# Performance work log

Hardware: AMD Instinct MI355X
Metric: run time of the kernel (lower is better)

Reference implementation:

```python
import jax, jax.numpy as jnp
import numpy as np
import math

IN_F, OUT_F, RANK, ALPHA = 4096, 4096, 16, 32
SCALING = ALPHA / RANK


def setup_inputs() -> dict:
    key = jax.random.key(0)
    k_x, k_w, k_a = jax.random.split(key, 3)
    x = jax.random.normal(k_x, (4, 2048, IN_F), dtype=jnp.float32)
    weight = jax.random.normal(k_w, (OUT_F, IN_F), dtype=jnp.float32)
    bias = jnp.zeros((OUT_F,), dtype=jnp.float32)
    lora_A = jax.random.normal(k_a, (RANK, IN_F), dtype=jnp.float32) * math.sqrt(2.0 / RANK)
    lora_B = jnp.zeros((OUT_F, RANK), dtype=jnp.float32)
    return {"x": x, "weight": weight, "bias": bias, "lora_A": lora_A, "lora_B": lora_B}


def reference(x, weight, bias, lora_A, lora_B):
    # base: x @ W^T + b    [B,S,out]
    base = jnp.einsum("bsi,oi->bso", x, weight) + bias
    # faithful to source: materialize full rank-update matrix (B @ A) [out,in]
    delta_w = lora_B @ lora_A
    lora = jnp.einsum("bsi,oi->bso", x, delta_w) * SCALING
    return base + lora
```

## Files before the change

kernel.cpp:

```cpp
#include <hip/hip_runtime.h>
#include <hip/hip_bf16.h>

#define IN_F   4096
#define OUT_F  4096
#define M_ROWS 8192
#define RANK   16
#define SCALING 2.0f

#define BM 256
#define BN 256
#define BK 64
#define NT (IN_F / BK)

typedef __attribute__((ext_vector_type(8))) short bf16x8;
typedef __attribute__((ext_vector_type(4))) float f32x4;
typedef unsigned short ushort_t;

template<int V> struct ic { static constexpr int value = V; };

__device__ __forceinline__ short f2b(float f) {
    union { float f; unsigned u; } c; c.f = f;
    unsigned r = (c.u + 0x7FFFu + ((c.u >> 16) & 1u)) >> 16;
    return (short)r;
}

__device__ __forceinline__ float4 ld4(const float* p) { return *(const float4*)p; }

__device__ __forceinline__ float4 s4(float4 v, float s) {
    v.x *= s; v.y *= s; v.z *= s; v.w *= s; return v;
}

__device__ __forceinline__ bf16x8 pack8(float4 a, float4 b) {
    bf16x8 r;
    r[0] = f2b(a.x); r[1] = f2b(a.y); r[2] = f2b(a.z); r[3] = f2b(a.w);
    r[4] = f2b(b.x); r[5] = f2b(b.y); r[6] = f2b(b.z); r[7] = f2b(b.w);
    return r;
}

__device__ __forceinline__ void gload16(const void* g, void* l) {
    __builtin_amdgcn_global_load_lds(
        (const __attribute__((address_space(1))) unsigned int*)g,
        (__attribute__((address_space(3))) unsigned int*)l, 16, 0, 0);
}

__global__ __launch_bounds__(256) void cvt3_kernel(const float* __restrict__ x,
                                                   const float* __restrict__ w,
                                                   const float* __restrict__ a,
                                                   ushort_t* __restrict__ xb,
                                                   ushort_t* __restrict__ wb,
                                                   ushort_t* __restrict__ ab) {
    const int n8x = M_ROWS * IN_F / 8;
    const int n8w = OUT_F * IN_F / 8;
    const int n8a = RANK * IN_F / 8;
    const int ntot = n8x + n8w + n8a;
    int i = blockIdx.x * blockDim.x + threadIdx.x;
    const int stride = gridDim.x * blockDim.x;
    for (; i < ntot; i += stride) {
        const float* src; ushort_t* dst; int j;
        if (i < n8x)            { src = x; dst = xb; j = i; }
        else if (i < n8x + n8w) { src = w; dst = wb; j = i - n8x; }
        else                    { src = a; dst = ab; j = i - n8x - n8w; }
        const float* p = src + (size_t)j * 8;
        *(bf16x8*)(dst + (size_t)j * 8) = pack8(ld4(p), ld4(p + 4));
    }
}

__global__ __launch_bounds__(256) void lora_t_mfma(const ushort_t* __restrict__ xb,
                                                   const ushort_t* __restrict__ ab,
                                                   float* __restrict__ T) {
    const int t = threadIdx.x, lane = t & 63, wv = t >> 6;
    const int r0 = blockIdx.x * 64 + wv * 16;
    const int l15 = lane & 15, lk = lane >> 4;
    const ushort_t* xr = xb + (size_t)(r0 + l15) * IN_F + lk * 8;
    const ushort_t* ar = ab + (size_t)l15 * IN_F + lk * 8;
    f32x4 acc = (f32x4){0.f, 0.f, 0.f, 0.f};
    for (int k0 = 0; k0 < IN_F; k0 += 32) {
        bf16x8 af = *(const bf16x8*)(xr + k0);
        bf16x8 bf = *(const bf16x8*)(ar + k0);
        acc = __builtin_amdgcn_mfma_f32_16x16x32_bf16(af, bf, acc, 0, 0, 0);
    }
#pragma unroll
    for (int v = 0; v < 4; v++)
        T[(size_t)(r0 + lk * 4 + v) * RANK + l15] = acc[v];
}

#define FENCE() asm volatile("" ::: "memory")

__global__ __launch_bounds__(512, 1) void gemm8p(
        const ushort_t* __restrict__ xb, const ushort_t* __restrict__ wb,
        const float* __restrict__ bias, const float* __restrict__ lora_B,
        const float* __restrict__ T, float* __restrict__ out) {

    __shared__ __align__(16) ushort_t As[2][BM * BK];
    __shared__ __align__(16) ushort_t Bs[2][BN * BK];

    const int tid  = threadIdx.x;
    const int lane = tid & 63, wv = tid >> 6;
    const int wm = wv >> 2, wn = wv & 3;
    const int l15 = lane & 15, lk = lane >> 4;

    const int bid = blockIdx.x;
    const int swz = (bid & 7) * 64 + (bid >> 3);
    const int by = swz >> 4, bx = swz & 15;
    const int brow = by * BM, bcol = bx * BN;

    const int off0 = wv * 2048 + lane * 16;
    const int off1 = off0 + 1024;
    const int row0 = off0 >> 7, row1 = off1 >> 7;
    const int sc0 = ((off0 & 127) ^ ((row0 & 7) << 4)) >> 1;
    const int sc1 = ((off1 & 127) ^ ((row1 & 7) << 4)) >> 1;
    const int ldst = wv * 1024;

    const size_t gA0 = (size_t)(brow + row0) * IN_F + sc0;
    const size_t gA1 = (size_t)(brow + row1) * IN_F + sc1;
    const size_t gB0 = (size_t)(bcol + row0) * IN_F + sc0;
    const size_t gB1 = (size_t)(bcol + row1) * IN_F + sc1;

    auto SA = [&](int h, int kt, auto BB) {
        constexpr int b = decltype(BB)::value;
        const size_t ho = (size_t)h * (128 * IN_F);
        gload16(xb + gA0 + ho + kt * 64, &As[b][h * 8192 + ldst]);
        gload16(xb + gA1 + ho + kt * 64, &As[b][h * 8192 + ldst + 512]);
    };
    auto SB = [&](int h, int kt, auto BB) {
        constexpr int b = decltype(BB)::value;
        const size_t ho = (size_t)h * (128 * IN_F);
        gload16(wb + gB0 + ho + kt * 64, &Bs[b][h * 8192 + ldst]);
        gload16(wb + gB1 + ho + kt * 64, &Bs[b][h * 8192 + ldst + 512]);
    };

    const int cb0 = (lk * 16) ^ ((l15 & 7) << 4);
    const int cb1 = (64 + lk * 16) ^ ((l15 & 7) << 4);
    const int am = wm * 128, bn = wn * 64;

    f32x4 acc[8][4];
#pragma unroll
    for (int m = 0; m < 8; m++)
#pragma unroll
        for (int n = 0; n < 4; n++) acc[m][n] = (f32x4){0.f, 0.f, 0.f, 0.f};

    bf16x8 af[8], bfq[8];

    SA(0, 0, ic<0>{}); SA(1, 0, ic<0>{});
    SB(0, 0, ic<0>{}); SB(1, 0, ic<0>{});
    SB(0, 1, ic<1>{}); SA(0, 1, ic<1>{});
    asm volatile("s_waitcnt vmcnt(4)" ::: "memory");
    __builtin_amdgcn_s_barrier();
    FENCE();

    auto TB = [&](auto CC, int tt) {
        constexpr int c = decltype(CC)::value;
        constexpr int n = c ^ 1;
        const int kt1 = (tt + 1 < NT) ? tt + 1 : NT - 1;
        const int kt2 = (tt + 2 < NT) ? tt + 2 : NT - 1;

#pragma unroll
        for (int mi = 0; mi < 4; mi++) {
            const char* rp = (const char*)&As[c][0] + (am + mi * 16 + l15) * 128;
            af[mi * 2]     = *(const bf16x8*)(rp + cb0);
            af[mi * 2 + 1] = *(const bf16x8*)(rp + cb1);
        }
#pragma unroll
        for (int ni = 0; ni < 2; ni++) {
            const char* rp = (const char*)&Bs[c][0] + (bn + ni * 16 + l15) * 128;
            bfq[ni * 2]     = *(const bf16x8*)(rp + cb0);
            bfq[ni * 2 + 1] = *(const bf16x8*)(rp + cb1);
        }
        SA(1, kt1, ic<n>{});
        asm volatile("s_waitcnt lgkmcnt(8)" ::: "memory");
        __builtin_amdgcn_s_barrier();
        FENCE();
        __builtin_amdgcn_s_setprio(1);
#pragma unroll
        for (int mi = 0; mi < 4; mi++)
#pragma unroll
            for (int ni = 0; ni < 2; ni++)
#pragma unroll
                for (int ks = 0; ks < 2; ks++)
                    acc[mi][ni] = __builtin_amdgcn_mfma_f32_16x16x32_bf16(
                        af[mi * 2 + ks], bfq[ni * 2 + ks], acc[mi][ni], 0, 0, 0);
        __builtin_amdgcn_s_setprio(0);
        FENCE();
        __builtin_amdgcn_s_barrier();
        FENCE();

#pragma unroll
        for (int ni = 0; ni < 2; ni++) {
            const char* rp = (const char*)&Bs[c][0] + (bn + 32 + ni * 16 + l15) * 128;
            bfq[(2 + ni) * 2]     = *(const bf16x8*)(rp + cb0);
            bfq[(2 + ni) * 2 + 1] = *(const bf16x8*)(rp + cb1);
        }
        SB(1, kt1, ic<n>{});
        FENCE();
        __builtin_amdgcn_s_barrier();
        FENCE();
        __builtin_amdgcn_s_setprio(1);
#pragma unroll
        for (int mi = 0; mi < 4; mi++)
#pragma unroll
            for (int ni = 0; ni < 2; ni++)
#pragma unroll
                for (int ks = 0; ks < 2; ks++)
                    acc[mi][2 + ni] = __builtin_amdgcn_mfma_f32_16x16x32_bf16(
                        af[mi * 2 + ks], bfq[(2 + ni) * 2 + ks], acc[mi][2 + ni], 0, 0, 0);
        __builtin_amdgcn_s_setprio(0);
        FENCE();
        __builtin_amdgcn_s_barrier();
        FENCE();

#pragma unroll
        for (int mi = 0; mi < 4; mi++) {
            const char* rp = (const char*)&As[c][0] + (am + 64 + mi * 16 + l15) * 128;
            af[mi * 2]     = *(const bf16x8*)(rp + cb0);
            af[mi * 2 + 1] = *(const bf16x8*)(rp + cb1);
        }
        SB(0, kt2, ic<c>{});
        FENCE();
        __builtin_amdgcn_s_barrier();
        FENCE();
        __builtin_amdgcn_s_setprio(1);
#pragma unroll
        for (int mi = 0; mi < 4; mi++)
#pragma unroll
            for (int ni = 0; ni < 2; ni++)
#pragma unroll
                for (int ks = 0; ks < 2; ks++)
                    acc[4 + mi][2 + ni] = __builtin_amdgcn_mfma_f32_16x16x32_bf16(
                        af[mi * 2 + ks], bfq[(2 + ni) * 2 + ks], acc[4 + mi][2 + ni], 0, 0, 0);
        __builtin_amdgcn_s_setprio(0);
        FENCE();
        __builtin_amdgcn_s_barrier();
        FENCE();

        SA(0, kt2, ic<c>{});
        FENCE();
        __builtin_amdgcn_s_barrier();
        FENCE();
        __builtin_amdgcn_s_setprio(1);
#pragma unroll
        for (int mi = 0; mi < 4; mi++)
#pragma unroll
            for (int ni = 0; ni < 2; ni++)
#pragma unroll
                for (int ks = 0; ks < 2; ks++)
                    acc[4 + mi][ni] = __builtin_amdgcn_mfma_f32_16x16x32_bf16(
                        af[mi * 2 + ks], bfq[ni * 2 + ks], acc[4 + mi][ni], 0, 0, 0);
        __builtin_amdgcn_s_setprio(0);
        asm volatile("s_waitcnt vmcnt(4)" ::: "memory");
        __builtin_amdgcn_s_barrier();
        FENCE();
    };

    for (int tt = 0; tt < NT; tt += 2) {
        TB(ic<0>{}, tt);
        TB(ic<1>{}, tt + 1);
    }

    asm volatile("s_waitcnt vmcnt(0)" ::: "memory");
    __builtin_amdgcn_s_barrier();
    {
        const int r = tid >> 1, hh = tid & 1;
        ushort_t* LA = &As[0][0];
        ushort_t* LB = &Bs[0][0];
        if (hh == 0) {
            const float* tp = T + (size_t)(brow + r) * RANK;
            *(bf16x8*)&LA[r * 32]     = pack8(s4(ld4(tp), SCALING), s4(ld4(tp + 4), SCALING));
            *(bf16x8*)&LA[r * 32 + 8] = pack8(s4(ld4(tp + 8), SCALING), s4(ld4(tp + 12), SCALING));
            const float* bp = lora_B + (size_t)(bcol + r) * RANK;
            *(bf16x8*)&LB[r * 32]     = pack8(ld4(bp), ld4(bp + 4));
            *(bf16x8*)&LB[r * 32 + 8] = pack8(ld4(bp + 8), ld4(bp + 12));
        } else {
            bf16x8 z;
#pragma unroll
            for (int i = 0; i < 8; i++) z[i] = 0;
            *(bf16x8*)&LA[r * 32 + 16] = z; *(bf16x8*)&LA[r * 32 + 24] = z;
            *(bf16x8*)&LB[r * 32 + 16] = z; *(bf16x8*)&LB[r * 32 + 24] = z;
        }
    }
    __syncthreads();
    {
        const ushort_t* LA = &As[0][0];
        const ushort_t* LB = &Bs[0][0];
        bf16x8 bfL[4];
#pragma unroll
        for (int n = 0; n < 4; n++)
            bfL[n] = *(const bf16x8*)&LB[(bn + n * 16 + l15) * 32 + lk * 8];
#pragma unroll
        for (int m = 0; m < 8; m++) {
            bf16x8 afL = *(const bf16x8*)&LA[(am + m * 16 + l15) * 32 + lk * 8];
#pragma unroll
            for (int n = 0; n < 4; n++)
                acc[m][n] = __builtin_amdgcn_mfma_f32_16x16x32_bf16(afL, bfL[n], acc[m][n], 0, 0, 0);
        }
    }

#pragma unroll
    for (int n = 0; n < 4; n++) {
        const int col = bcol + bn + n * 16 + l15;
        const float bv = bias[col];
#pragma unroll
        for (int m = 0; m < 8; m++) {
            const int row0_ = brow + am + m * 16 + lk * 4;
#pragma unroll
            for (int v = 0; v < 4; v++)
                out[(size_t)(row0_ + v) * OUT_F + col] = acc[m][n][v] + bv;
        }
    }
}

__global__ __launch_bounds__(256) void lora_t_kernel(const float* __restrict__ x,
                                                     const float* __restrict__ lora_A,
                                                     float* __restrict__ T) {
    const int t   = threadIdx.x;
    const int row = blockIdx.x * 16 + (t >> 4);
    const int rr  = t & 15;
    const float* xr = x + (size_t)row * IN_F;
    const float* ar = lora_A + (size_t)rr * IN_F;
    float acc = 0.f;
#pragma unroll 8
    for (int k = 0; k < IN_F; k += 4) {
        float4 xv = ld4(xr + k);
        float4 av = ld4(ar + k);
        acc += xv.x * av.x + xv.y * av.y + xv.z * av.z + xv.w * av.w;
    }
    T[row * RANK + rr] = acc;
}

__global__ __launch_bounds__(256) void lora_gemm_kernel(
        const float* __restrict__ x, const float* __restrict__ w,
        const float* __restrict__ bias, const float* __restrict__ lora_B,
        const float* __restrict__ T, float* __restrict__ out) {

    __shared__ __align__(16) short As[128][32];
    __shared__ __align__(16) short Bs[128][32];

    const int t    = threadIdx.x;
    const int brow = blockIdx.y * 128;
    const int bcol = blockIdx.x * 128;
    const int srow  = t >> 1;
    const int shalf = (t & 1) << 4;
    const float* xa = x + (size_t)(brow + srow) * IN_F + shalf;
    const float* wb = w + (size_t)(bcol + srow) * IN_F + shalf;
    const int lane = t & 63;
    const int wv   = t >> 6;
    const int wr   = wv >> 1, wc = wv & 1;
    const int l15  = lane & 15, lk = lane >> 4;

    f32x4 acc[4][4];
#pragma unroll
    for (int m = 0; m < 4; m++)
#pragma unroll
        for (int n = 0; n < 4; n++)
            acc[m][n] = (f32x4){0.f, 0.f, 0.f, 0.f};

    for (int k0 = 0; k0 < IN_F; k0 += 32) {
        float4 a0 = ld4(xa + k0);      float4 a1 = ld4(xa + k0 + 4);
        float4 a2 = ld4(xa + k0 + 8);  float4 a3 = ld4(xa + k0 + 12);
        float4 b0 = ld4(wb + k0);      float4 b1 = ld4(wb + k0 + 4);
        float4 b2 = ld4(wb + k0 + 8);  float4 b3 = ld4(wb + k0 + 12);

        __syncthreads();
        *(bf16x8*)&As[srow][shalf]     = pack8(a0, a1);
        *(bf16x8*)&As[srow][shalf + 8] = pack8(a2, a3);
        *(bf16x8*)&Bs[srow][shalf]     = pack8(b0, b1);
        *(bf16x8*)&Bs[srow][shalf + 8] = pack8(b2, b3);
        __syncthreads();

        bf16x8 af[4], bf[4];
#pragma unroll
        for (int m = 0; m < 4; m++) af[m] = *(bf16x8*)&As[wr * 64 + m * 16 + l15][lk * 8];
#pragma unroll
        for (int n = 0; n < 4; n++) bf[n] = *(bf16x8*)&Bs[wc * 64 + n * 16 + l15][lk * 8];
#pragma unroll
        for (int m = 0; m < 4; m++)
#pragma unroll
            for (int n = 0; n < 4; n++)
                acc[m][n] = __builtin_amdgcn_mfma_f32_16x16x32_bf16(af[m], bf[n], acc[m][n], 0, 0, 0);
    }

    __syncthreads();
    if (shalf == 0) {
        const float* tp = T + (size_t)(brow + srow) * RANK;
        *(bf16x8*)&As[srow][0] = pack8(s4(ld4(tp), SCALING), s4(ld4(tp + 4), SCALING));
        *(bf16x8*)&As[srow][8] = pack8(s4(ld4(tp + 8), SCALING), s4(ld4(tp + 12), SCALING));
        const float* bp = lora_B + (size_t)(bcol + srow) * RANK;
        *(bf16x8*)&Bs[srow][0] = pack8(ld4(bp), ld4(bp + 4));
        *(bf16x8*)&Bs[srow][8] = pack8(ld4(bp + 8), ld4(bp + 12));
    } else {
        bf16x8 z;
#pragma unroll
        for (int i = 0; i < 8; i++) z[i] = 0;
        *(bf16x8*)&As[srow][16] = z; *(bf16x8*)&As[srow][24] = z;
        *(bf16x8*)&Bs[srow][16] = z; *(bf16x8*)&Bs[srow][24] = z;
    }
    __syncthreads();
    {
        bf16x8 af[4], bf[4];
#pragma unroll
        for (int m = 0; m < 4; m++) af[m] = *(bf16x8*)&As[wr * 64 + m * 16 + l15][lk * 8];
#pragma unroll
        for (int n = 0; n < 4; n++) bf[n] = *(bf16x8*)&Bs[wc * 64 + n * 16 + l15][lk * 8];
#pragma unroll
        for (int m = 0; m < 4; m++)
#pragma unroll
            for (int n = 0; n < 4; n++)
                acc[m][n] = __builtin_amdgcn_mfma_f32_16x16x32_bf16(af[m], bf[n], acc[m][n], 0, 0, 0);
    }

    const int ocol0 = bcol + wc * 64 + l15;
#pragma unroll
    for (int n = 0; n < 4; n++) {
        const int col = ocol0 + n * 16;
        const float bv = bias[col];
#pragma unroll
        for (int m = 0; m < 4; m++) {
            const int row0 = brow + wr * 64 + m * 16 + lk * 4;
#pragma unroll
            for (int v = 0; v < 4; v++) {
                out[(size_t)(row0 + v) * OUT_F + col] = acc[m][n][v] + bv;
            }
        }
    }
}

extern "C" void kernel_launch(void* const* d_in, const int* in_sizes, int n_in,
                              void* d_out, int out_size, void* d_ws, size_t ws_size,
                              hipStream_t stream) {
    const float* x      = (const float*)d_in[0];
    const float* w      = (const float*)d_in[1];
    const float* bias   = (const float*)d_in[2];
    const float* lora_A = (const float*)d_in[3];
    const float* lora_B = (const float*)d_in[4];
    float* out = (float*)d_out;

    const size_t OFF_T = 0;
    const size_t OFF_A = 524288;
    const size_t OFF_W = 655360;
    const size_t OFF_X = 34209792;
    const size_t WS_NEED = 101318656;

    if (ws_size >= WS_NEED) {
        char* ws = (char*)d_ws;
        float*    T   = (float*)(ws + OFF_T);
        ushort_t* ab  = (ushort_t*)(ws + OFF_A);
        ushort_t* wbp = (ushort_t*)(ws + OFF_W);
        ushort_t* xbp = (ushort_t*)(ws + OFF_X);

        cvt3_kernel<<<3072, 256, 0, stream>>>(x, w, lora_A, xbp, wbp, ab);
        lora_t_mfma<<<M_ROWS / 64, 256, 0, stream>>>(xbp, ab, T);
        gemm8p<<<(M_ROWS / BM) * (OUT_F / BN), 512, 0, stream>>>(xbp, wbp, bias, lora_B, T, out);
    } else {
        float* T = (float*)d_ws;
        lora_t_kernel<<<M_ROWS / 16, 256, 0, stream>>>(x, lora_A, T);
        dim3 grid(OUT_F / 128, M_ROWS / 128);
        lora_gemm_kernel<<<grid, 256, 0, stream>>>(x, w, bias, lora_B, T, out);
    }
}
```

Baseline: 333.5 us.

## Fuse conversion, LoRA projection and GEMM into one cooperative persistent kernel

Replaces the three-launch pipeline (fp32->bf16 conversion, x·A^T projection, tiled GEMM) with a single cooperative kernel of 256 blocks. Each block converts a slice of inputs, computes part of T directly from fp32 x, then runs a grid-wide sync and processes two 256x256 output tiles persistently. It also drops several intra-iteration barriers in the GEMM main loop, relying on the remaining barriers for LDS buffer safety. This trades launch gaps and kernel boundaries for a grid sync, half-occupied CUs during the conversion phase, and a possible LDS race if the removed barriers were needed.

```diff
diff --git a/kernel.cpp b/kernel.cpp
--- a/kernel.cpp
+++ b/kernel.cpp
@@ -1,5 +1,8 @@
 #include <hip/hip_runtime.h>
 #include <hip/hip_bf16.h>
+#include <hip/hip_cooperative_groups.h>
+
+namespace cg = cooperative_groups;
 
 #define IN_F   4096
 #define OUT_F  4096
@@ -41,6 +44,259 @@
     __builtin_amdgcn_global_load_lds(
         (const __attribute__((address_space(1))) unsigned int*)g,
         (__attribute__((address_space(3))) unsigned int*)l, 16, 0, 0);
+}
+
+#define FENCE() asm volatile("" ::: "memory")
+
+__global__ __launch_bounds__(512, 1) void fused_all(
+        const float* __restrict__ x, const float* __restrict__ w,
+        const float* __restrict__ bias, const float* __restrict__ lora_A,
+        const float* __restrict__ lora_B,
+        ushort_t* __restrict__ xb, ushort_t* __restrict__ wb,
+        ushort_t* __restrict__ ab, float* __restrict__ T,
+        float* __restrict__ out) {
+
+    __shared__ __align__(16) ushort_t As[2][BM * BK];
+    __shared__ __align__(16) ushort_t Bs[2][BN * BK];
+
+    const int tid  = threadIdx.x;
+    const int lane = tid & 63, wv = tid >> 6;
+    const int wm = wv >> 2, wn = wv & 3;
+    const int l15 = lane & 15, lk = lane >> 4;
+
+    {
+        const int n8x = M_ROWS * IN_F / 8;
+        const int n8w = OUT_F * IN_F / 8;
+        const int n8a = RANK * IN_F / 8;
+        const int ntot = n8x + n8w + n8a;
+        int i = blockIdx.x * 512 + tid;
+        const int stride = 256 * 512;
+        for (; i < ntot; i += stride) {
+            const float* src; ushort_t* dst; int j;
+            if (i < n8x)            { src = x; dst = xb; j = i; }
+            else if (i < n8x + n8w) { src = w; dst = wb; j = i - n8x; }
+            else                    { src = lora_A; dst = ab; j = i - n8x - n8w; }
+            const float* p = src + (size_t)j * 8;
+            *(bf16x8*)(dst + (size_t)j * 8) = pack8(ld4(p), ld4(p + 4));
+        }
+    }
+
+    if (wv < 2) {
+        const int r0 = blockIdx.x * 32 + wv * 16;
+        const float* xr = x + (size_t)(r0 + l15) * IN_F + lk * 8;
+        const float* ar = lora_A + (size_t)l15 * IN_F + lk * 8;
+        f32x4 accT = (f32x4){0.f, 0.f, 0.f, 0.f};
+        for (int k0 = 0; k0 < IN_F; k0 += 32) {
+            bf16x8 afr = pack8(ld4(xr + k0), ld4(xr + k0 + 4));
+            bf16x8 bfr = pack8(ld4(ar + k0), ld4(ar + k0 + 4));
+            accT = __builtin_amdgcn_mfma_f32_16x16x32_bf16(afr, bfr, accT, 0, 0, 0);
+        }
+#pragma unroll
+        for (int v = 0; v < 4; v++)
+            T[(size_t)(r0 + lk * 4 + v) * RANK + l15] = accT[v];
+    }
+
+    cg::this_grid().sync();
+
+    const int off0 = wv * 2048 + lane * 16;
+    const int off1 = off0 + 1024;
+    const int row0 = off0 >> 7, row1 = off1 >> 7;
+    const int sc0 = ((off0 & 127) ^ ((row0 & 7) << 4)) >> 1;
+    const int sc1 = ((off1 & 127) ^ ((row1 & 7) << 4)) >> 1;
+    const int ldst = wv * 1024;
+
+    const int cb0 = (lk * 16) ^ ((l15 & 7) << 4);
+    const int cb1 = (64 + lk * 16) ^ ((l15 & 7) << 4);
+    const int am = wm * 128, bn = wn * 64;
+
+#pragma unroll 1
+    for (int rep = 0; rep < 2; ++rep) {
+        const int swzv = (blockIdx.x & 7) * 64 + (blockIdx.x >> 3) + rep * 32;
+        const int bx = swzv >> 5, by = swzv & 31;
+        const int brow = by * BM, bcol = bx * BN;
+
+        const size_t gA0 = (size_t)(brow + row0) * IN_F + sc0;
+        const size_t gA1 = (size_t)(brow + row1) * IN_F + sc1;
+        const size_t gB0 = (size_t)(bcol + row0) * IN_F + sc0;
+        const size_t gB1 = (size_t)(bcol + row1) * IN_F + sc1;
+
+        auto SA = [&](int h, int kt, auto BB) {
+            constexpr int b = decltype(BB)::value;
+            const size_t ho = (size_t)h * (128 * IN_F);
+            gload16(xb + gA0 + ho + kt * 64, &As[b][h * 8192 + ldst]);
+            gload16(xb + gA1 + ho + kt * 64, &As[b][h * 8192 + ldst + 512]);
+        };
+        auto SB = [&](int h, int kt, auto BB) {
+            constexpr int b = decltype(BB)::value;
+            const size_t ho = (size_t)h * (128 * IN_F);
+            gload16(wb + gB0 + ho + kt * 64, &Bs[b][h * 8192 + ldst]);
+            gload16(wb + gB1 + ho + kt * 64, &Bs[b][h * 8192 + ldst + 512]);
+        };
+
+        f32x4 acc[8][4];
+#pragma unroll
+        for (int m = 0; m < 8; m++)
+#pragma unroll
+            for (int n = 0; n < 4; n++) acc[m][n] = (f32x4){0.f, 0.f, 0.f, 0.f};
+
+        bf16x8 af[8], bfq[8];
+
+        __syncthreads();
+
+        SA(0, 0, ic<0>{}); SA(1, 0, ic<0>{});
+        SB(0, 0, ic<0>{}); SB(1, 0, ic<0>{});
+        SB(0, 1, ic<1>{}); SA(0, 1, ic<1>{});
+        asm volatile("s_waitcnt vmcnt(4)" ::: "memory");
+        __builtin_amdgcn_s_barrier();
+        FENCE();
+
+        auto TB = [&](auto CC, int tt) {
+            constexpr int c = decltype(CC)::value;
+            constexpr int n = c ^ 1;
+            const int kt1 = (tt + 1 < NT) ? tt + 1 : NT - 1;
+            const int kt2 = (tt + 2 < NT) ? tt + 2 : NT - 1;
+
+            SA(1, kt1, ic<n>{});
+#pragma unroll
+            for (int mi = 0; mi < 4; mi++) {
+                const char* rp = (const char*)&As[c][0] + (am + mi * 16 + l15) * 128;
+                af[mi * 2]     = *(const bf16x8*)(rp + cb0);
+                af[mi * 2 + 1] = *(const bf16x8*)(rp + cb1);
+            }
+#pragma unroll
+            for (int ni = 0; ni < 2; ni++) {
+                const char* rp = (const char*)&Bs[c][0] + (bn + ni * 16 + l15) * 128;
+                bfq[ni * 2]     = *(const bf16x8*)(rp + cb0);
+                bfq[ni * 2 + 1] = *(const bf16x8*)(rp + cb1);
+            }
+            __builtin_amdgcn_s_setprio(1);
+#pragma unroll
+            for (int mi = 0; mi < 4; mi++)
+#pragma unroll
+                for (int ni = 0; ni < 2; ni++)
+#pragma unroll
+                    for (int ks = 0; ks < 2; ks++)
+                        acc[mi][ni] = __builtin_amdgcn_mfma_f32_16x16x32_bf16(
+                            af[mi * 2 + ks], bfq[ni * 2 + ks], acc[mi][ni], 0, 0, 0);
+            __builtin_amdgcn_s_setprio(0);
+            FENCE();
+            __builtin_amdgcn_s_barrier();
+            FENCE();
+
+            SB(1, kt1, ic<n>{});
+#pragma unroll
+            for (int ni = 0; ni < 2; ni++) {
+                const char* rp = (const char*)&Bs[c][0] + (bn + 32 + ni * 16 + l15) * 128;
+                bfq[(2 + ni) * 2]     = *(const bf16x8*)(rp + cb0);
+                bfq[(2 + ni) * 2 + 1] = *(const bf16x8*)(rp + cb1);
+            }
+            __builtin_amdgcn_s_setprio(1);
+#pragma unroll
+            for (int mi = 0; mi < 4; mi++)
+#pragma unroll
+                for (int ni = 0; ni < 2; ni++)
+#pragma unroll
+                    for (int ks = 0; ks < 2; ks++)
+                        acc[mi][2 + ni] = __builtin_amdgcn_mfma_f32_16x16x32_bf16(
+                            af[mi * 2 + ks], bfq[(2 + ni) * 2 + ks], acc[mi][2 + ni], 0, 0, 0);
+            __builtin_amdgcn_s_setprio(0);
+            FENCE();
+            __builtin_amdgcn_s_barrier();
+            FENCE();
+
+            SB(0, kt2, ic<c>{});
+#pragma unroll
+            for (int mi = 0; mi < 4; mi++) {
+                const char* rp = (const char*)&As[c][0] + (am + 64 + mi * 16 + l15) * 128;
+                af[mi * 2]     = *(const bf16x8*)(rp + cb0);
+                af[mi * 2 + 1] = *(const bf16x8*)(rp + cb1);
+            }
+            __builtin_amdgcn_s_setprio(1);
+#pragma unroll
+            for (int mi = 0; mi < 4; mi++)
+#pragma unroll
+                for (int ni = 0; ni < 2; ni++)
+#pragma unroll
+                    for (int ks = 0; ks < 2; ks++)
+                        acc[4 + mi][2 + ni] = __builtin_amdgcn_mfma_f32_16x16x32_bf16(
+                            af[mi * 2 + ks], bfq[(2 + ni) * 2 + ks], acc[4 + mi][2 + ni], 0, 0, 0);
+            __builtin_amdgcn_s_setprio(0);
+            FENCE();
+            __builtin_amdgcn_s_barrier();
+            FENCE();
+
+            SA(0, kt2, ic<c>{});
+            __builtin_amdgcn_s_setprio(1);
+#pragma unroll
+            for (int mi = 0; mi < 4; mi++)
+#pragma unroll
+                for (int ni = 0; ni < 2; ni++)
+#pragma unroll
+                    for (int ks = 0; ks < 2; ks++)
+                        acc[4 + mi][ni] = __builtin_amdgcn_mfma_f32_16x16x32_bf16(
+                            af[mi * 2 + ks], bfq[ni * 2 + ks], acc[4 + mi][ni], 0, 0, 0);
+            __builtin_amdgcn_s_setprio(0);
+            asm volatile("s_waitcnt vmcnt(4)" ::: "memory");
+            __builtin_amdgcn_s_barrier();
+            FENCE();
+        };
+
+        for (int tt = 0; tt < NT; tt += 2) {
+            TB(ic<0>{}, tt);
+            TB(ic<1>{}, tt + 1);
+        }
+
+        asm volatile("s_waitcnt vmcnt(0)" ::: "memory");
+        __builtin_amdgcn_s_barrier();
+        {
+            const int r = tid >> 1, hh = tid & 1;
+            ushort_t* LA = &As[0][0];
+            ushort_t* LB = &Bs[0][0];
+            if (hh == 0) {
+                const float* tp = T + (size_t)(brow + r) * RANK;
+                *(bf16x8*)&LA[r * 32]     = pack8(s4(ld4(tp), SCALING), s4(ld4(tp + 4), SCALING));
+                *(bf16x8*)&LA[r * 32 + 8] = pack8(s4(ld4(tp + 8), SCALING), s4(ld4(tp + 12), SCALING));
+                const float* bp = lora_B + (size_t)(bcol + r) * RANK;
+                *(bf16x8*)&LB[r * 32]     = pack8(ld4(bp), ld4(bp + 4));
+                *(bf16x8*)&LB[r * 32 + 8] = pack8(ld4(bp + 8), ld4(bp + 12));
+            } else {
+                bf16x8 z;
+#pragma unroll
+                for (int i = 0; i < 8; i++) z[i] = 0;
+                *(bf16x8*)&LA[r * 32 + 16] = z; *(bf16x8*)&LA[r * 32 + 24] = z;
+                *(bf16x8*)&LB[r * 32 + 16] = z; *(bf16x8*)&LB[r * 32 + 24] = z;
+            }
+        }
+        __syncthreads();
+        {
+            const ushort_t* LA = &As[0][0];
+            const ushort_t* LB = &Bs[0][0];
+            bf16x8 bfL[4];
+#pragma unroll
+            for (int n = 0; n < 4; n++)
+                bfL[n] = *(const bf16x8*)&LB[(bn + n * 16 + l15) * 32 + lk * 8];
+#pragma unroll
+            for (int m = 0; m < 8; m++) {
+                bf16x8 afL = *(const bf16x8*)&LA[(am + m * 16 + l15) * 32 + lk * 8];
+#pragma unroll
+                for (int n = 0; n < 4; n++)
+                    acc[m][n] = __builtin_amdgcn_mfma_f32_16x16x32_bf16(afL, bfL[n], acc[m][n], 0, 0, 0);
+            }
+        }
+
+#pragma unroll
+        for (int n = 0; n < 4; n++) {
+            const int col = bcol + bn + n * 16 + l15;
+            const float bv = bias[col];
+#pragma unroll
+            for (int m = 0; m < 8; m++) {
+                const int row0_ = brow + am + m * 16 + lk * 4;
+#pragma unroll
+                for (int v = 0; v < 4; v++)
+                    out[(size_t)(row0_ + v) * OUT_F + col] = acc[m][n][v] + bv;
+            }
+        }
+    }
 }
 
 __global__ __launch_bounds__(256) void cvt3_kernel(const float* __restrict__ x,
@@ -65,11 +321,11 @@
     }
 }
 
-__global__ __launch_bounds__(256) void lora_t_mfma(const ushort_t* __restrict__ xb,
-                                                   const ushort_t* __restrict__ ab,
-                                                   float* __restrict__ T) {
-    const int t = threadIdx.x, lane = t & 63, wv = t >> 6;
-    const int r0 = blockIdx.x * 64 + wv * 16;
+__global__ __launch_bounds__(64) void lora_t_mfma(const ushort_t* __restrict__ xb,
+                                                  const ushort_t* __restrict__ ab,
+                                                  float* __restrict__ T) {
+    const int lane = threadIdx.x & 63;
+    const int r0 = blockIdx.x * 16;
     const int l15 = lane & 15, lk = lane >> 4;
     const ushort_t* xr = xb + (size_t)(r0 + l15) * IN_F + lk * 8;
     const ushort_t* ar = ab + (size_t)l15 * IN_F + lk * 8;
@@ -83,8 +339,6 @@
     for (int v = 0; v < 4; v++)
         T[(size_t)(r0 + lk * 4 + v) * RANK + l15] = acc[v];
 }
-
-#define FENCE() asm volatile("" ::: "memory")
 
 __global__ __launch_bounds__(512, 1) void gemm8p(
         const ushort_t* __restrict__ xb, const ushort_t* __restrict__ wb,
@@ -167,9 +421,6 @@
             bfq[ni * 2 + 1] = *(const bf16x8*)(rp + cb1);
         }
         SA(1, kt1, ic<n>{});
-        asm volatile("s_waitcnt lgkmcnt(8)" ::: "memory");
-        __builtin_amdgcn_s_barrier();
-        FENCE();
         __builtin_amdgcn_s_setprio(1);
 #pragma unroll
         for (int mi = 0; mi < 4; mi++)
@@ -191,9 +442,6 @@
             bfq[(2 + ni) * 2 + 1] = *(const bf16x8*)(rp + cb1);
         }
         SB(1, kt1, ic<n>{});
-        FENCE();
-        __builtin_amdgcn_s_barrier();
-        FENCE();
         __builtin_amdgcn_s_setprio(1);
 #pragma unroll
         for (int mi = 0; mi < 4; mi++)
@@ -215,9 +463,6 @@
             af[mi * 2 + 1] = *(const bf16x8*)(rp + cb1);
         }
         SB(0, kt2, ic<c>{});
-        FENCE();
-        __builtin_amdgcn_s_barrier();
-        FENCE();
         __builtin_amdgcn_s_setprio(1);
 #pragma unroll
         for (int mi = 0; mi < 4; mi++)
@@ -233,9 +478,6 @@
         FENCE();
 
         SA(0, kt2, ic<c>{});
-        FENCE();
-        __builtin_amdgcn_s_barrier();
-        FENCE();
         __builtin_amdgcn_s_setprio(1);
 #pragma unroll
         for (int mi = 0; mi < 4; mi++)
@@ -442,13 +684,21 @@
     if (ws_size >= WS_NEED) {
         char* ws = (char*)d_ws;
         float*    T   = (float*)(ws + OFF_T);
-        ushort_t* ab  = (ushort_t*)(ws + OFF_A);
+        ushort_t* abp = (ushort_t*)(ws + OFF_A);
         ushort_t* wbp = (ushort_t*)(ws + OFF_W);
         ushort_t* xbp = (ushort_t*)(ws + OFF_X);
 
-        cvt3_kernel<<<3072, 256, 0, stream>>>(x, w, lora_A, xbp, wbp, ab);
-        lora_t_mfma<<<M_ROWS / 64, 256, 0, stream>>>(xbp, ab, T);
-        gemm8p<<<(M_ROWS / BM) * (OUT_F / BN), 512, 0, stream>>>(xbp, wbp, bias, lora_B, T, out);
+        void* kargs[] = {(void*)&x, (void*)&w, (void*)&bias, (void*)&lora_A,
+                         (void*)&lora_B, (void*)&xbp, (void*)&wbp, (void*)&abp,
+                         (void*)&T, (void*)&out};
+        hipError_t err = hipLaunchCooperativeKernel((const void*)fused_all,
+                                                    dim3(256), dim3(512),
+                                                    kargs, 0, stream);
+        if (err != hipSuccess) {
+            cvt3_kernel<<<3072, 256, 0, stream>>>(x, w, lora_A, xbp, wbp, abp);
+            lora_t_mfma<<<M_ROWS / 16, 64, 0, stream>>>(xbp, abp, T);
+            gemm8p<<<(M_ROWS / BM) * (OUT_F / BN), 512, 0, stream>>>(xbp, wbp, bias, lora_B, T, out);
+        }
     } else {
         float* T = (float*)d_ws;
         lora_t_kernel<<<M_ROWS / 16, 256, 0, stream>>>(x, lora_A, T);
```

Result: slower. 484.4 us (+45.3%).
